# Kernel optimization log

Measured on AMD Instinct MI355X. Metric: run time of the kernel, lower is better.

Reference implementation:

```python
import jax, jax.numpy as jnp
import numpy as np


def setup_inputs() -> dict:
    key = jax.random.key(0)
    k1, k2 = jax.random.split(key)
    queries = jax.random.normal(k1, (16, 1024, 256), dtype=jnp.float32)
    embedding = jax.random.normal(k2, (8192, 256), dtype=jnp.float32) * 0.02
    return {"queries": queries, "embedding": embedding}


def reference(queries, embedding):
    commitment_weight = 0.25
    # squared L2 distances: ||q||^2 + ||e||^2 - 2 q.e  -> [b, k, n]
    q_sq = jnp.sum(queries * queries, axis=-1, keepdims=True)          # [b,k,1]
    e_sq = jnp.sum(embedding * embedding, axis=-1)[None, None, :]      # [1,1,n]
    distances = q_sq + e_sq - 2.0 * jnp.einsum('bkc,nc->bkn', queries, embedding)
    code_indices = jnp.argmin(distances, axis=-1)                      # [b,k] int
    quantized = embedding[code_indices]                                # [b,k,c]
    commit_loss = jnp.mean((jax.lax.stop_gradient(queries) - quantized) ** 2)
    codebook_loss = jnp.mean((queries - jax.lax.stop_gradient(quantized)) ** 2)
    vq_loss = codebook_loss + commitment_weight * commit_loss
    # straight-through estimator
    quantized_st = queries + jax.lax.stop_gradient(quantized - queries)
    return (code_indices, quantized_st, vq_loss)
```

## Files before the change

kernel.cpp:

```cpp
#include <hip/hip_runtime.h>
#include <float.h>

typedef _Float16 half8 __attribute__((ext_vector_type(8)));
typedef _Float16 half4v __attribute__((ext_vector_type(4)));
typedef float f32x4 __attribute__((ext_vector_type(4)));

#define M_TOTAL 16384
#define N_CODES 8192
#define KDIM    256
#define BM 128
#define BN 256
#define BK 32
#define NK (KDIM / BK)
#define NB (N_CODES / BN)
#define TS 32
#define MARGIN 3.6e-3f
#define SQ_SCALE 512.0f
#define SE_SCALE 2048.0f
#define INV_PROD 1.9073486328125e-06f
#define RG 4
#define RCODES 1024
#define RNCH (N_CODES / RCODES)
#define RPB 1024
#define RM_BLOCKS 256
#define LR_BLOCKS 32

#define PREP_Q_BLOCKS (M_TOTAL / 4)
#define PREP_E_BLOCKS (N_CODES / 4)
#define TR_BLOCKS ((N_CODES / 64) * (KDIM / 64))

__device__ __forceinline__ void prep_body(const float* __restrict__ src,
                                          _Float16* __restrict__ dst,
                                          float* __restrict__ sq, float scale,
                                          int row0, int tid) {
    {
        const int r = row0 + (tid >> 6);
        const int e4 = tid & 63;
        const float4 v = *(const float4*)(src + (size_t)r * KDIM + e4 * 4);
        const half4v h = {(_Float16)(v.x * scale), (_Float16)(v.y * scale),
                          (_Float16)(v.z * scale), (_Float16)(v.w * scale)};
        ((half4v*)(dst + (size_t)r * KDIM))[e4] = h;
    }
    if (tid < 64) {
        const int grp = tid >> 4;
        const int sub = tid & 15;
        const int row = row0 + grp;
        const float* p = src + (size_t)row * KDIM + (sub >> 3) * 128 + (sub & 7);
        float r;
        {
            #pragma clang fp contract(off)
            float v = p[0];
            r = v * v;
            #pragma unroll
            for (int k = 1; k < 16; k++) { const float w = p[k * 8]; r = r + w * w; }
        }
        const float t1 = r  + __shfl_xor(r,  1, 64);
        const float t2 = t1 + __shfl_xor(t1, 2, 64);
        const float t3 = t2 + __shfl_xor(t2, 4, 64);
        const float t4 = t3 + __shfl_xor(t3, 8, 64);
        if (sub == 0) sq[row] = t4;
    }
}

__global__ void prep_fused_kernel(const float* __restrict__ Q, const float* __restrict__ E,
                                  _Float16* __restrict__ Qh, _Float16* __restrict__ Eh,
                                  float* __restrict__ qsq, float* __restrict__ esq,
                                  float* __restrict__ ET) {
    __shared__ float tile[64][65];
    const int tid = threadIdx.x;
    const int b = blockIdx.x;
    if (b < PREP_Q_BLOCKS) {
        prep_body(Q, Qh, qsq, SQ_SCALE, b * 4, tid);
        return;
    }
    if (b < PREP_Q_BLOCKS + PREP_E_BLOCKS) {
        prep_body(E, Eh, esq, SE_SCALE, (b - PREP_Q_BLOCKS) * 4, tid);
        return;
    }
    const int idx = b - PREP_Q_BLOCKS - PREP_E_BLOCKS;
    const int n0 = (idx & 127) * 64;
    const int k0 = (idx >> 7) * 64;
    const int r = tid >> 4;
    const int c4 = tid & 15;
    #pragma unroll
    for (int p = 0; p < 4; p++) {
        const int row = p * 16 + r;
        const float4 v = *(const float4*)(E + (size_t)(n0 + row) * KDIM + k0 + c4 * 4);
        tile[row][c4 * 4 + 0] = v.x;
        tile[row][c4 * 4 + 1] = v.y;
        tile[row][c4 * 4 + 2] = v.z;
        tile[row][c4 * 4 + 3] = v.w;
    }
    __syncthreads();
    #pragma unroll
    for (int p = 0; p < 4; p++) {
        const int d = p * 16 + r;
        float4 o;
        o.x = tile[c4 * 4 + 0][d];
        o.y = tile[c4 * 4 + 1][d];
        o.z = tile[c4 * 4 + 2][d];
        o.w = tile[c4 * 4 + 3][d];
        *(float4*)(ET + (size_t)(k0 + d) * N_CODES + n0 + c4 * 4) = o;
    }
}

union SMemU {
    struct { _Float16 q[3][BM * TS]; _Float16 e[3][BN * TS]; } t;
    struct { unsigned k1[BM][2]; unsigned k2[BM][2]; } red;
};

__device__ __forceinline__ void gl_lds16(const void* g, void* lds) {
    __builtin_amdgcn_global_load_lds(
        (const __attribute__((address_space(1))) unsigned*)g,
        (__attribute__((address_space(3))) unsigned*)lds, 16, 0, 0);
}

__global__ __launch_bounds__(256, 2)
void mfma_top2_kernel(const _Float16* __restrict__ Qh, const _Float16* __restrict__ Eh,
                      const float* __restrict__ esq,
                      unsigned* __restrict__ k1s, unsigned* __restrict__ k2s) {
    __shared__ SMemU sm;
    const int tid = threadIdx.x;
    const int m0 = blockIdx.x * BM;
    const int n0 = blockIdx.y * BN;
    const int w = tid >> 6, lane = tid & 63;
    const int wm = w >> 1, wn = w & 1;
    const int qd = lane >> 4, c = lane & 15;

    const int lrow = lane >> 2;
    const int gsw = (lane & 3) ^ ((lane >> 3) & 3);
    const _Float16* qsrc = Qh + (size_t)(m0 + w * 32 + lrow) * KDIM + gsw * 8;
    const _Float16* esrc = Eh + (size_t)(n0 + w * 64 + lrow) * KDIM + gsw * 8;

    f32x4 acc[4][8];
    const f32x4 zero = {0.f, 0.f, 0.f, 0.f};
    #pragma unroll
    for (int mt = 0; mt < 4; mt++)
        #pragma unroll
        for (int nt = 0; nt < 8; nt++) acc[mt][nt] = zero;

    #define STAGE(buf, kofs) do {                                                  \
        _Float16* qdst = sm.t.q[buf] + w * 1024;                                   \
        _Float16* edst = sm.t.e[buf] + w * 2048;                                   \
        gl_lds16(qsrc + (kofs),             qdst);                                 \
        gl_lds16(qsrc + 16 * KDIM + (kofs), qdst + 512);                           \
        gl_lds16(esrc + (kofs),             edst);                                 \
        gl_lds16(esrc + 16 * KDIM + (kofs), edst + 512);                           \
        gl_lds16(esrc + 32 * KDIM + (kofs), edst + 1024);                          \
        gl_lds16(esrc + 48 * KDIM + (kofs), edst + 1536);                          \
    } while (0)

    STAGE(0, 0);
    STAGE(1, BK);
    STAGE(2, 2 * BK);
    asm volatile("s_waitcnt vmcnt(12)" ::: "memory");
    __builtin_amdgcn_s_barrier();

    const int csw = (c >> 1) & 3;

    #pragma unroll
    for (int ki = 0; ki < NK; ki++) {
        const int buf = ki % 3;
        const _Float16* bq = sm.t.q[buf];
        const _Float16* be = sm.t.e[buf];
        half8 qa[4];
        #pragma unroll
        for (int mt = 0; mt < 4; mt++)
            qa[mt] = *(const half8*)(bq + (wm * 64 + mt * 16 + c) * TS + (qd ^ csw) * 8);
        __builtin_amdgcn_s_setprio(1);
        #pragma unroll
        for (int nt = 0; nt < 8; nt++) {
            const half8 eh = *(const half8*)(be + (wn * 128 + nt * 16 + c) * TS + (qd ^ csw) * 8);
            #pragma unroll
            for (int mt = 0; mt < 4; mt++)
                acc[mt][nt] = __builtin_amdgcn_mfma_f32_16x16x32_f16(qa[mt], eh, acc[mt][nt], 0, 0, 0);
        }
        __builtin_amdgcn_s_setprio(0);
        if (ki == NK - 1) break;
        if (ki <= NK - 3) { asm volatile("s_waitcnt vmcnt(6)" ::: "memory"); }
        else              { asm volatile("s_waitcnt vmcnt(0)" ::: "memory"); }
        __builtin_amdgcn_s_barrier();
        if (ki + 3 < NK) STAGE(buf, (ki + 3) * BK);
    }
    #undef STAGE

    float es8[8];
    #pragma unroll
    for (int nt = 0; nt < 8; nt++) es8[nt] = esq[n0 + wn * 128 + nt * 16 + c] + 8.0f;

    unsigned k1[16], k2[16];
    #pragma unroll
    for (int i = 0; i < 16; i++) { k1[i] = 0xFFFFFFFFu; k2[i] = 0xFFFFFFFFu; }

    #pragma unroll
    for (int mt = 0; mt < 4; mt++)
        #pragma unroll
        for (int nt = 0; nt < 8; nt++) {
            const unsigned nl = (unsigned)(wn * 128 + nt * 16 + c);
            #pragma unroll
            for (int r = 0; r < 4; r++) {
                const int i = mt * 4 + r;
                const float d = fmaf(acc[mt][nt][r], -INV_PROD, es8[nt]);
                const unsigned k = (__float_as_uint(d) & 0xFFFFFF00u) | nl;
                const unsigned t = min(k1[i], k);
                k2[i] = min(k2[i], max(k1[i], k));
                k1[i] = t;
            }
        }
    #pragma unroll
    for (int s = 1; s < 16; s <<= 1) {
        #pragma unroll
        for (int i = 0; i < 16; i++) {
            const unsigned ok1 = (unsigned)__shfl_xor((int)k1[i], s, 64);
            const unsigned ok2 = (unsigned)__shfl_xor((int)k2[i], s, 64);
            const unsigned t = min(k1[i], ok1);
            k2[i] = min(min(k2[i], ok2), max(k1[i], ok1));
            k1[i] = t;
        }
    }
    __syncthreads();
    if (c == 0) {
        #pragma unroll
        for (int mt = 0; mt < 4; mt++)
            #pragma unroll
            for (int r = 0; r < 4; r++) {
                const int ml = wm * 64 + mt * 16 + qd * 4 + r;
                sm.red.k1[ml][wn] = k1[mt * 4 + r];
                sm.red.k2[ml][wn] = k2[mt * 4 + r];
            }
    }
    __syncthreads();
    if (tid < BM) {
        const unsigned a1 = sm.red.k1[tid][0], b1 = sm.red.k1[tid][1];
        const unsigned a2 = sm.red.k2[tid][0], b2 = sm.red.k2[tid][1];
        const size_t o = (size_t)(m0 + tid) * NB + blockIdx.y;
        k1s[o] = min(a1, b1);
        k2s[o] = min(min(a2, b2), max(a1, b1));
    }
}

__global__ void finalize_kernel(const float* __restrict__ Q, const float* __restrict__ E,
                                const unsigned* __restrict__ k1s, const unsigned* __restrict__ k2s,
                                int* __restrict__ fcount, int* __restrict__ flist,
                                float* __restrict__ ws_loss, float* __restrict__ out) {
    const int q = blockIdx.x * 4 + (threadIdx.x >> 6);
    const int lane = threadIdx.x & 63;
    unsigned d1 = 0xFFFFFF00u;
    unsigned d2 = 0xFFFFFF00u;
    int gi = 0x7FFFFFFF;
    if (lane < NB) {
        const unsigned k1 = k1s[(size_t)q * NB + lane];
        const unsigned k2 = k2s[(size_t)q * NB + lane];
        d1 = k1 & 0xFFFFFF00u;
        gi = lane * BN + (int)(k1 & 255u);
        d2 = k2 & 0xFFFFFF00u;
    }
    #pragma unroll
    for (int s = 1; s < 64; s <<= 1) {
        const unsigned od1 = (unsigned)__shfl_xor((int)d1, s, 64);
        const int      ogi = __shfl_xor(gi, s, 64);
        const unsigned od2 = (unsigned)__shfl_xor((int)d2, s, 64);
        const unsigned nd2 = min(min(d2, od2), max(d1, od1));
        const bool take = (od1 < d1) || (od1 == d1 && ogi < gi);
        d1 = take ? od1 : d1;
        gi = take ? ogi : gi;
        d2 = nd2;
    }
    if ((__uint_as_float(d2) - __uint_as_float(d1)) < MARGIN) {
        if (lane == 0) flist[atomicAdd(fcount, 1)] = q;
        return;
    }

    if (lane == 0) out[q] = (float)gi;
    const float4 qv = *(const float4*)(Q + (size_t)q * KDIM + lane * 4);
    const float4 ev = *(const float4*)(E + (size_t)gi * KDIM + lane * 4);
    float4 st;
    {
        #pragma clang fp contract(off)
        st.x = qv.x + (ev.x - qv.x);
        st.y = qv.y + (ev.y - qv.y);
        st.z = qv.z + (ev.z - qv.z);
        st.w = qv.w + (ev.w - qv.w);
    }
    *(float4*)(out + M_TOTAL + (size_t)q * KDIM + lane * 4) = st;

    const float dx = qv.x - ev.x, dy = qv.y - ev.y, dz = qv.z - ev.z, dw = qv.w - ev.w;
    float s = dx * dx + dy * dy + dz * dz + dw * dw;
    #pragma unroll
    for (int off = 32; off > 0; off >>= 1) s += __shfl_down(s, off);
    if (lane == 0) ws_loss[q] = s;
}

__global__ __launch_bounds__(256, 4)
void refine_partial_kernel(const float* __restrict__ Q, const float* __restrict__ ET,
                           const float* __restrict__ qsq, const float* __restrict__ esq,
                           const int* __restrict__ fcount, const int* __restrict__ flist,
                           float* __restrict__ rp_v, int* __restrict__ rp_i) {
    const int cnt = *fcount;
    if (cnt == 0) return;
    const int ngroups = (cnt + RG - 1) / RG;
    const int ntasks = ngroups * RNCH;
    const int tid = threadIdx.x;
    const int w = tid >> 6, lane = tid & 63;
    __shared__ float qs[RG][KDIM];
    __shared__ float redv[4][RG];
    __shared__ int   redi[4][RG];

    for (int t = blockIdx.x; t < ntasks; t += RPB) {
        const int grp = t >> 3;
        const int chunk = t & (RNCH - 1);
        __syncthreads();
        {
            const int g = tid >> 6, c4 = tid & 63;
            const int fi = min(grp * RG + g, cnt - 1);
            const int q = flist[fi];
            *(float4*)&qs[g][c4 * 4] = *(const float4*)(Q + (size_t)q * KDIM + c4 * 4);
        }
        __syncthreads();

        const int nb = chunk * RCODES + tid * 4;
        float a[RG][4];
        #pragma unroll
        for (int g = 0; g < RG; g++)
            #pragma unroll
            for (int j = 0; j < 4; j++) a[g][j] = 0.f;

        for (int k4 = 0; k4 < KDIM / 4; k4++) {
            float4 qv[RG];
            #pragma unroll
            for (int g = 0; g < RG; g++) qv[g] = *(const float4*)&qs[g][k4 * 4];
            #pragma unroll
            for (int kk = 0; kk < 4; kk++) {
                const float4 ev = *(const float4*)(ET + (size_t)(k4 * 4 + kk) * N_CODES + nb);
                #pragma unroll
                for (int g = 0; g < RG; g++) {
                    const float qk = (kk == 0) ? qv[g].x : (kk == 1) ? qv[g].y
                                   : (kk == 2) ? qv[g].z : qv[g].w;
                    a[g][0] = fmaf(qk, ev.x, a[g][0]);
                    a[g][1] = fmaf(qk, ev.y, a[g][1]);
                    a[g][2] = fmaf(qk, ev.z, a[g][2]);
                    a[g][3] = fmaf(qk, ev.w, a[g][3]);
                }
            }
        }

        float es[4];
        #pragma unroll
        for (int j = 0; j < 4; j++) es[j] = esq[nb + j];

        #pragma unroll
        for (int g = 0; g < RG; g++) {
            const int fi = min(grp * RG + g, cnt - 1);
            const float qsv = qsq[flist[fi]];
            float bv = FLT_MAX; int bi = 0x7fffffff;
            #pragma unroll
            for (int j = 0; j < 4; j++) {
                float d;
                {
                    #pragma clang fp contract(off)
                    const float t1 = qsv + es[j];
                    d = t1 - 2.0f * a[g][j];
                }
                if (d < bv) { bv = d; bi = nb + j; }
            }
            #pragma unroll
            for (int s = 1; s < 64; s <<= 1) {
                const float ov = __shfl_xor(bv, s, 64);
                const int   oi = __shfl_xor(bi, s, 64);
                if (ov < bv || (ov == bv && oi < bi)) { bv = ov; bi = oi; }
            }
            if (lane == 0) { redv[w][g] = bv; redi[w][g] = bi; }
        }
        __syncthreads();
        if (tid < RG) {
            float fv = redv[0][tid]; int fidx = redi[0][tid];
            #pragma unroll
            for (int u = 1; u < 4; u++) {
                if (redv[u][tid] < fv || (redv[u][tid] == fv && redi[u][tid] < fidx)) {
                    fv = redv[u][tid]; fidx = redi[u][tid];
                }
            }
            rp_v[(size_t)t * RG + tid] = fv;
            rp_i[(size_t)t * RG + tid] = fidx;
        }
    }
}

__global__ void refine_merge_kernel(const float* __restrict__ Q, const float* __restrict__ E,
                                    const int* __restrict__ fcount, const int* __restrict__ flist,
                                    const float* __restrict__ rp_v, const int* __restrict__ rp_i,
                                    float* __restrict__ ws_loss, float* __restrict__ out) {
    const int cnt = *fcount;
    const int lane = threadIdx.x;
    for (int fi = blockIdx.x; fi < cnt; fi += RM_BLOCKS) {
        const int q = flist[fi];
        const int grp = fi >> 2, g = fi & 3;
        float bv = FLT_MAX; int bi = 0x7fffffff;
        if (lane < RNCH) {
            const size_t t = (size_t)(grp * RNCH + lane);
            bv = rp_v[t * RG + g];
            bi = rp_i[t * RG + g];
        }
        #pragma unroll
        for (int s = 1; s < 64; s <<= 1) {
            const float ov = __shfl_xor(bv, s, 64);
            const int   oi = __shfl_xor(bi, s, 64);
            if (ov < bv || (ov == bv && oi < bi)) { bv = ov; bi = oi; }
        }
        if (lane == 0) out[q] = (float)bi;

        const float4 qv = *(const float4*)(Q + (size_t)q * KDIM + lane * 4);
        const float4 ev = *(const float4*)(E + (size_t)bi * KDIM + lane * 4);
        float4 st;
        {
            #pragma clang fp contract(off)
            st.x = qv.x + (ev.x - qv.x);
            st.y = qv.y + (ev.y - qv.y);
            st.z = qv.z + (ev.z - qv.z);
            st.w = qv.w + (ev.w - qv.w);
        }
        *(float4*)(out + M_TOTAL + (size_t)q * KDIM + lane * 4) = st;
        const float dx = qv.x - ev.x, dy = qv.y - ev.y, dz = qv.z - ev.z, dw = qv.w - ev.w;
        float s = dx * dx + dy * dy + dz * dz + dw * dw;
        #pragma unroll
        for (int off = 32; off > 0; off >>= 1) s += __shfl_down(s, off);
        if (lane == 0) ws_loss[q] = s;
    }
}

__global__ void loss_reduce_kernel(const float* __restrict__ ws_loss, float* __restrict__ out) {
    const int tid = threadIdx.x;
    float s = 0.f;
    for (int i = blockIdx.x * 256 + tid; i < M_TOTAL; i += LR_BLOCKS * 256)
        s += ws_loss[i];
    #pragma unroll
    for (int off = 32; off > 0; off >>= 1) s += __shfl_down(s, off);
    __shared__ float ws[4];
    if ((tid & 63) == 0) ws[tid >> 6] = s;
    __syncthreads();
    if (tid == 0) {
        const float tot = (ws[0] + ws[1]) + (ws[2] + ws[3]);
        atomicAdd(out + M_TOTAL + (size_t)M_TOTAL * KDIM,
                  tot * (1.25f / (float)((size_t)M_TOTAL * KDIM)));
    }
}

extern "C" void kernel_launch(void* const* d_in, const int* in_sizes, int n_in,
                              void* d_out, int out_size, void* d_ws, size_t ws_size,
                              hipStream_t stream) {
    const float* Q = (const float*)d_in[0];
    const float* E = (const float*)d_in[1];
    float* out = (float*)d_out;

    char* ws = (char*)d_ws;
    _Float16* Qh  = (_Float16*)(ws);
    _Float16* Eh  = (_Float16*)(ws + (size_t)8  * 1024 * 1024);
    float* qsq    = (float*)   (ws + (size_t)12 * 1024 * 1024);
    float* esq    = qsq + M_TOTAL;
    unsigned* k1s = (unsigned*)(ws + (size_t)13 * 1024 * 1024);
    unsigned* k2s = (unsigned*)(ws + (size_t)17 * 1024 * 1024);
    int*   fcount = (int*)     (ws + (size_t)25 * 1024 * 1024);
    int*   flist  = fcount + 64;
    float* ws_loss= (float*)   (ws + (size_t)25 * 1024 * 1024 + 512 * 1024);
    float* ET     = (float*)   (ws + (size_t)26 * 1024 * 1024);
    float* rp_v   = (float*)k1s;
    int*   rp_i   = (int*)k2s;

    hipMemsetAsync(out + M_TOTAL + (size_t)M_TOTAL * KDIM, 0, sizeof(float), stream);
    hipMemsetAsync(fcount, 0, sizeof(int), stream);

    prep_fused_kernel<<<PREP_Q_BLOCKS + PREP_E_BLOCKS + TR_BLOCKS, 256, 0, stream>>>(
        Q, E, Qh, Eh, qsq, esq, ET);

    mfma_top2_kernel<<<dim3(M_TOTAL / BM, N_CODES / BN), 256, 0, stream>>>(
        Qh, Eh, esq, k1s, k2s);

    finalize_kernel<<<M_TOTAL / 4, 256, 0, stream>>>(Q, E, k1s, k2s, fcount, flist, ws_loss, out);
    refine_partial_kernel<<<RPB, 256, 0, stream>>>(Q, ET, qsq, esq, fcount, flist, rp_v, rp_i);
    refine_merge_kernel<<<RM_BLOCKS, 64, 0, stream>>>(Q, E, fcount, flist, rp_v, rp_i, ws_loss, out);
    loss_reduce_kernel<<<LR_BLOCKS, 256, 0, stream>>>(ws_loss, out);
}
```

Measured before the change: 216.9 us.

## Fold memsets into prep kernel, hoist esq loads, split MFMA loop with barriers

Removes the two hipMemsetAsync calls by zeroing the fail counter and loss slot inside the prep kernel, which saves two stream operations. In the MFMA kernel, the esq loads now happen before the main loop so their latency overlaps the pipeline prologue. The inner K loop is split into two halves, each loading E fragments up front, with extra s_barrier calls between halves to keep the waves in lockstep. The added barriers and the extra live registers could cost occupancy or stall time.

```diff
diff --git a/kernel.cpp b/kernel.cpp
--- a/kernel.cpp
+++ b/kernel.cpp
@@ -65,10 +65,12 @@
 __global__ void prep_fused_kernel(const float* __restrict__ Q, const float* __restrict__ E,
                                   _Float16* __restrict__ Qh, _Float16* __restrict__ Eh,
                                   float* __restrict__ qsq, float* __restrict__ esq,
-                                  float* __restrict__ ET) {
+                                  float* __restrict__ ET,
+                                  int* __restrict__ fcount, float* __restrict__ loss_slot) {
     __shared__ float tile[64][65];
     const int tid = threadIdx.x;
     const int b = blockIdx.x;
+    if (b == 0 && tid == 0) { *fcount = 0; *loss_slot = 0.f; }
     if (b < PREP_Q_BLOCKS) {
         prep_body(Q, Qh, qsq, SQ_SCALE, b * 4, tid);
         return;
@@ -153,6 +155,11 @@
     STAGE(0, 0);
     STAGE(1, BK);
     STAGE(2, 2 * BK);
+
+    float es8[8];
+    #pragma unroll
+    for (int nt = 0; nt < 8; nt++) es8[nt] = esq[n0 + wn * 128 + nt * 16 + c] + 8.0f;
+
     asm volatile("s_waitcnt vmcnt(12)" ::: "memory");
     __builtin_amdgcn_s_barrier();
 
@@ -163,19 +170,37 @@
         const int buf = ki % 3;
         const _Float16* bq = sm.t.q[buf];
         const _Float16* be = sm.t.e[buf];
+
         half8 qa[4];
         #pragma unroll
         for (int mt = 0; mt < 4; mt++)
             qa[mt] = *(const half8*)(bq + (wm * 64 + mt * 16 + c) * TS + (qd ^ csw) * 8);
+        half8 eh[4];
+        #pragma unroll
+        for (int nt = 0; nt < 4; nt++)
+            eh[nt] = *(const half8*)(be + (wn * 128 + nt * 16 + c) * TS + (qd ^ csw) * 8);
+        __builtin_amdgcn_s_barrier();
         __builtin_amdgcn_s_setprio(1);
         #pragma unroll
-        for (int nt = 0; nt < 8; nt++) {
-            const half8 eh = *(const half8*)(be + (wn * 128 + nt * 16 + c) * TS + (qd ^ csw) * 8);
+        for (int nt = 0; nt < 4; nt++)
             #pragma unroll
             for (int mt = 0; mt < 4; mt++)
-                acc[mt][nt] = __builtin_amdgcn_mfma_f32_16x16x32_f16(qa[mt], eh, acc[mt][nt], 0, 0, 0);
-        }
+                acc[mt][nt] = __builtin_amdgcn_mfma_f32_16x16x32_f16(qa[mt], eh[nt], acc[mt][nt], 0, 0, 0);
         __builtin_amdgcn_s_setprio(0);
+
+        half8 eh2[4];
+        #pragma unroll
+        for (int nt = 0; nt < 4; nt++)
+            eh2[nt] = *(const half8*)(be + (wn * 128 + (nt + 4) * 16 + c) * TS + (qd ^ csw) * 8);
+        __builtin_amdgcn_s_barrier();
+        __builtin_amdgcn_s_setprio(1);
+        #pragma unroll
+        for (int nt = 0; nt < 4; nt++)
+            #pragma unroll
+            for (int mt = 0; mt < 4; mt++)
+                acc[mt][nt + 4] = __builtin_amdgcn_mfma_f32_16x16x32_f16(qa[mt], eh2[nt], acc[mt][nt + 4], 0, 0, 0);
+        __builtin_amdgcn_s_setprio(0);
+
         if (ki == NK - 1) break;
         if (ki <= NK - 3) { asm volatile("s_waitcnt vmcnt(6)" ::: "memory"); }
         else              { asm volatile("s_waitcnt vmcnt(0)" ::: "memory"); }
@@ -183,10 +208,6 @@
         if (ki + 3 < NK) STAGE(buf, (ki + 3) * BK);
     }
     #undef STAGE
-
-    float es8[8];
-    #pragma unroll
-    for (int nt = 0; nt < 8; nt++) es8[nt] = esq[n0 + wn * 128 + nt * 16 + c] + 8.0f;
 
     unsigned k1[16], k2[16];
     #pragma unroll
@@ -465,12 +486,10 @@
     float* ET     = (float*)   (ws + (size_t)26 * 1024 * 1024);
     float* rp_v   = (float*)k1s;
     int*   rp_i   = (int*)k2s;
-
-    hipMemsetAsync(out + M_TOTAL + (size_t)M_TOTAL * KDIM, 0, sizeof(float), stream);
-    hipMemsetAsync(fcount, 0, sizeof(int), stream);
+    float* loss_slot = out + M_TOTAL + (size_t)M_TOTAL * KDIM;
 
     prep_fused_kernel<<<PREP_Q_BLOCKS + PREP_E_BLOCKS + TR_BLOCKS, 256, 0, stream>>>(
-        Q, E, Qh, Eh, qsq, esq, ET);
+        Q, E, Qh, Eh, qsq, esq, ET, fcount, loss_slot);
 
     mfma_top2_kernel<<<dim3(M_TOTAL / BM, N_CODES / BN), 256, 0, stream>>>(
         Qh, Eh, esq, k1s, k2s);
```

Measured after the change: 226.8 us. 1.05x slower.
